# Kernel optimization log

Measured on AMD Instinct MI355X. Metric: run time of the kernel, lower is better.

The kernel has to match this reference:

```python
import jax, jax.numpy as jnp
import numpy as np

N = 500_000
K = 16
E = N * K
H = 256


def _linear_params(key, fan_in, fan_out):
    k1, k2 = jax.random.split(key)
    bound = 1.0 / np.sqrt(fan_in)
    W = jax.random.uniform(k1, (fan_in, fan_out), jnp.float32, -bound, bound)
    b = jax.random.uniform(k2, (fan_out,), jnp.float32, -bound, bound)
    return W, b


def setup_inputs() -> dict:
    key = jax.random.key(0)
    ks = jax.random.split(key, 10)
    x = jax.random.normal(ks[0], (N, 3), jnp.float32)
    edge_index = jax.random.randint(ks[1], (2, E), 0, N, jnp.int64)
    edge_attr = jax.random.normal(ks[2], (E, 1), jnp.float32)
    W1, b1 = _linear_params(ks[3], K, H)          # GNN1 message MLP: Linear(k, 256)
    We1, be1 = _linear_params(ks[4], H, 128)      # encoder Linear(256,128)
    We2, be2 = _linear_params(ks[5], 128, 6)      # encoder Linear(128,6)
    Wd1, bd1 = _linear_params(ks[6], 6, 128)      # decoder Linear(6,128)
    Wd2, bd2 = _linear_params(ks[7], 128, H)      # decoder Linear(128,256)
    Wo, bo = _linear_params(ks[8], H, 1)          # output Linear(256,1)
    return {"x": x, "edge_index": edge_index, "edge_attr": edge_attr,
            "W1": W1, "b1": b1, "We1": We1, "be1": be1, "We2": We2, "be2": be2,
            "Wd1": Wd1, "bd1": bd1, "Wd2": Wd2, "bd2": bd2, "Wo": Wo, "bo": bo}


def reference(x, edge_index, edge_attr, W1, b1, We1, be1, We2, be2,
              Wd1, bd1, Wd2, bd2, Wo, bo):
    # GNN1: messages are edge_attr verbatim (x_i/x_j ignored); aggregate reshapes
    # all E scalar messages into (N, k) (k edges per node, contiguous) and runs
    # Linear(k,256)+Tanh. Note: LSTM and GCN4 branches in the torch code are dead
    # (GNN1 ignores its node-feature input), so they do not affect the output.
    k = W1.shape[0]
    msgs = edge_attr.reshape(-1, k)                    # (N, k)
    h = jnp.tanh(msgs @ W1 + b1)                       # (N, 256)
    # second L1 call produces the identical result (depends only on edge_attr)
    z = jnp.tanh(jnp.tanh(h @ We1 + be1) @ We2 + be2)  # encoder -> (N, 6)
    d = jnp.tanh(z @ Wd1 + bd1) @ Wd2 + bd2            # decoder -> (N, 256)
    out = jax.nn.sigmoid(jnp.tanh(d) @ Wo + bo)        # (N, 1)
    return out[:, 0]                                   # squeeze(dim=1) -> (N,)
```

## Files before the change

kernel.cpp:

```cpp
#include <hip/hip_runtime.h>


#define N_NODES 500000

#define OFF_W1 0
#define OFF_W2 8192
#define OFF_W3 73728
#define OFF_W4 77824
#define OFF_W5 86016
#define OFF_WO 151552
#define OFF_B1 152576
#define OFF_B2 153600
#define OFF_B3 154112
#define OFF_B4 154176
#define OFF_B5 154688
#define IMG_BYTES 155712
#define IMG_ALLOC 156672

#define K1_LDS   79872
#define K1_B1    77824
#define K1_B2    78848
#define K1_B3    79360
#define K2_LDS   76800
#define K2_W4    0
#define K2_W5    8192
#define K2_WO    73728
#define K2_B4    74752
#define K2_B5    75264

typedef _Float16 half8  __attribute__((ext_vector_type(8)));
typedef __fp16   pk16x2 __attribute__((ext_vector_type(2)));
typedef float    f32x4  __attribute__((ext_vector_type(4)));
typedef int      int4v  __attribute__((ext_vector_type(4)));

__device__ __align__(16) char g_img[IMG_ALLOC];

static __device__ __forceinline__ unsigned pack_f16_rne(float a, float b) {
  _Float16 ha = (_Float16)a, hb = (_Float16)b;
  unsigned short ua = __builtin_bit_cast(unsigned short, ha);
  unsigned short ub = __builtin_bit_cast(unsigned short, hb);
  return (unsigned)ua | ((unsigned)ub << 16);
}
static __device__ __forceinline__ int pkrtz(float a, float b) {
  pk16x2 h = __builtin_amdgcn_cvt_pkrtz(a, b);
  return __builtin_bit_cast(int, h);
}
static __device__ __forceinline__ float tanh_f(float x) {
  float e = __builtin_amdgcn_exp2f(x * 2.8853900817779268f);
  float r = __builtin_amdgcn_rcpf(e + 1.0f);
  return __builtin_fmaf(-2.0f, r, 1.0f);
}
static __device__ __forceinline__ float sigmoid_f(float x) {
  float e = __builtin_amdgcn_exp2f(x * -1.4426950408889634f);
  return __builtin_amdgcn_rcpf(1.0f + e);
}
static __device__ __forceinline__ f32x4 mfma16(half8 a, int4v b, f32x4 c) {
  return __builtin_amdgcn_mfma_f32_16x16x32_f16(a, __builtin_bit_cast(half8, b), c, 0, 0, 0);
}
static __device__ __forceinline__ half8 lda(const char* smem, int off) {
  return *(const half8*)(smem + off);
}
static __device__ __forceinline__ f32x4 ldf4(const char* smem, int off) {
  return *(const f32x4*)(smem + off);
}
#define FENCE() __builtin_amdgcn_sched_barrier(0)

struct PK2 { int lo, hi; };
static __device__ __forceinline__ PK2 tp(f32x4 a) {
  PK2 p;
  p.lo = pkrtz(tanh_f(a.x), tanh_f(a.y));
  p.hi = pkrtz(tanh_f(a.z), tanh_f(a.w));
  return p;
}
static __device__ __forceinline__ int4v xform(PK2 e, PK2 o, int s1, int s2, bool qlo) {
  int x0 = __shfl(e.lo, s1, 64), y0 = __shfl(o.lo, s1, 64);
  int x1 = __shfl(e.hi, s1, 64), y1 = __shfl(o.hi, s1, 64);
  int x2 = __shfl(e.lo, s2, 64), y2 = __shfl(o.lo, s2, 64);
  int x3 = __shfl(e.hi, s2, 64), y3 = __shfl(o.hi, s2, 64);
  int4v r;
  r.x = qlo ? x0 : y0;  r.y = qlo ? x1 : y1;
  r.z = qlo ? x2 : y2;  r.w = qlo ? x3 : y3;
  return r;
}

__global__ void gnn_prep(const float* __restrict__ W1,  const float* __restrict__ b1,
                         const float* __restrict__ We1, const float* __restrict__ be1,
                         const float* __restrict__ We2, const float* __restrict__ be2,
                         const float* __restrict__ Wd1, const float* __restrict__ bd1,
                         const float* __restrict__ Wd2, const float* __restrict__ bd2,
                         const float* __restrict__ Wo)
{
  int t = blockIdx.x * 256 + threadIdx.x;
  int off = t * 4;
  if (off >= IMG_BYTES) return;
  unsigned val;
  if (off < OFF_W2) {
    int rel = off;
    int mi = rel >> 9, li = (rel >> 4) & 31, j2 = (rel >> 2) & 3;
    int fout = mi * 16 + (li & 15);
    int k0 = (li >> 4) * 8 + j2 * 2;
    val = pack_f16_rne(W1[k0 * 256 + fout], W1[(k0 + 1) * 256 + fout]);
  } else if (off < OFF_W3) {
    int rel = off - OFF_W2;
    int blk = rel >> 10, li = (rel >> 4) & 63, j2 = (rel >> 2) & 3;
    int mi = blk >> 3, ki = blk & 7;
    int fout = mi * 16 + (li & 15);
    int k0 = ki * 32 + (li >> 4) * 8 + j2 * 2;
    val = pack_f16_rne(We1[k0 * 128 + fout], We1[(k0 + 1) * 128 + fout]);
  } else if (off < OFF_W4) {
    int rel = off - OFF_W3;
    int ki = rel >> 10, li = (rel >> 4) & 63, j2 = (rel >> 2) & 3;
    int fo = li & 15;
    int k0 = ki * 32 + (li >> 4) * 8 + j2 * 2;
    float a = (fo < 6) ? We2[k0 * 6 + fo] : 0.0f;
    float b = (fo < 6) ? We2[(k0 + 1) * 6 + fo] : 0.0f;
    val = pack_f16_rne(a, b);
  } else if (off < OFF_W5) {
    int rel = off - OFF_W4;
    int mi = rel >> 10, li = (rel >> 4) & 63, j2 = (rel >> 2) & 3;
    int fout = mi * 16 + (li & 15);
    int k0 = (li >> 4) * 8 + j2 * 2;
    float a = (k0 < 6)     ? Wd1[k0 * 128 + fout]       : 0.0f;
    float b = (k0 + 1 < 6) ? Wd1[(k0 + 1) * 128 + fout] : 0.0f;
    val = pack_f16_rne(a, b);
  } else if (off < OFF_WO) {
    int rel = off - OFF_W5;
    int blk = rel >> 10, li = (rel >> 4) & 63, j2 = (rel >> 2) & 3;
    int mi = blk >> 2, ki = blk & 3;
    int fout = mi * 16 + (li & 15);
    int k0 = ki * 32 + (li >> 4) * 8 + j2 * 2;
    val = pack_f16_rne(Wd2[k0 * 256 + fout], Wd2[(k0 + 1) * 256 + fout]);
  } else if (off < OFF_B1) {
    val = __builtin_bit_cast(unsigned, Wo[(off - OFF_WO) >> 2]);
  } else if (off < OFF_B2) {
    val = __builtin_bit_cast(unsigned, b1[(off - OFF_B1) >> 2]);
  } else if (off < OFF_B3) {
    val = __builtin_bit_cast(unsigned, be1[(off - OFF_B2) >> 2]);
  } else if (off < OFF_B4) {
    int i = (off - OFF_B3) >> 2;
    float v = (i < 6) ? be2[i] : 0.0f;
    val = __builtin_bit_cast(unsigned, v);
  } else if (off < OFF_B5) {
    val = __builtin_bit_cast(unsigned, bd1[(off - OFF_B4) >> 2]);
  } else {
    val = __builtin_bit_cast(unsigned, bd2[(off - OFF_B5) >> 2]);
  }
  *(unsigned*)(g_img + off) = val;
}

static __device__ __forceinline__ void stage_chunk(const char* src, char* dst) {
  __builtin_amdgcn_global_load_lds(
      (const __attribute__((address_space(1))) void*)src,
      (__attribute__((address_space(3))) void*)dst, 16, 0, 0);
}

#define L1_PAIR(KO, OUT_G0, OUT_G1) do {                                   \
    half8 Ae = lda(smem, OFF_W1 + (2*(KO))*512 + (ln & 31)*16);            \
    half8 Ao = lda(smem, OFF_W1 + (2*(KO)+1)*512 + (ln & 31)*16);          \
    if (!qlo) { Ae = h8z; Ao = h8z; }                                      \
    f32x4 be_ = ldf4(smem, K1_B1 + (2*(KO))*64 + q*16);                    \
    f32x4 bo_ = ldf4(smem, K1_B1 + (2*(KO)+1)*64 + q*16);                  \
    f32x4 ae0 = mfma16(Ae, b1g0, be_);                                     \
    f32x4 ae1 = mfma16(Ae, b1g1, be_);                                     \
    f32x4 ao0 = mfma16(Ao, b1g0, bo_);                                     \
    f32x4 ao1 = mfma16(Ao, b1g1, bo_);                                     \
    PK2 pe0 = tp(ae0), po0 = tp(ao0), pe1 = tp(ae1), po1 = tp(ao1);        \
    OUT_G0 = xform(pe0, po0, s1, s2, qlo);                                 \
    OUT_G1 = xform(pe1, po1, s1, s2, qlo);                                 \
    FENCE();                                                               \
  } while (0)

#define L2_MI(MI, ACC0, ACC1) do {                                                            \
    f32x4 bb = ldf4(smem, K1_B2 + (MI)*64 + q*16);                                            \
    ACC0 = bb; ACC1 = bb;                                                                     \
    half8 A;                                                                                  \
    A = lda(smem, OFF_W2 + ((MI)*8+0)*1024 + ln*16); ACC0 = mfma16(A, c2g0_0, ACC0); ACC1 = mfma16(A, c2g1_0, ACC1); \
    A = lda(smem, OFF_W2 + ((MI)*8+1)*1024 + ln*16); ACC0 = mfma16(A, c2g0_1, ACC0); ACC1 = mfma16(A, c2g1_1, ACC1); \
    A = lda(smem, OFF_W2 + ((MI)*8+2)*1024 + ln*16); ACC0 = mfma16(A, c2g0_2, ACC0); ACC1 = mfma16(A, c2g1_2, ACC1); \
    A = lda(smem, OFF_W2 + ((MI)*8+3)*1024 + ln*16); ACC0 = mfma16(A, c2g0_3, ACC0); ACC1 = mfma16(A, c2g1_3, ACC1); \
    A = lda(smem, OFF_W2 + ((MI)*8+4)*1024 + ln*16); ACC0 = mfma16(A, c2g0_4, ACC0); ACC1 = mfma16(A, c2g1_4, ACC1); \
    A = lda(smem, OFF_W2 + ((MI)*8+5)*1024 + ln*16); ACC0 = mfma16(A, c2g0_5, ACC0); ACC1 = mfma16(A, c2g1_5, ACC1); \
    A = lda(smem, OFF_W2 + ((MI)*8+6)*1024 + ln*16); ACC0 = mfma16(A, c2g0_6, ACC0); ACC1 = mfma16(A, c2g1_6, ACC1); \
    A = lda(smem, OFF_W2 + ((MI)*8+7)*1024 + ln*16); ACC0 = mfma16(A, c2g0_7, ACC0); ACC1 = mfma16(A, c2g1_7, ACC1); \
  } while (0)

#define L2_PAIR(KO, OUT_G0, OUT_G1) do {                                   \
    f32x4 ve0, ve1, vo0, vo1;                                              \
    L2_MI(2*(KO),   ve0, ve1);                                             \
    FENCE();                                                               \
    L2_MI(2*(KO)+1, vo0, vo1);                                             \
    PK2 pe0 = tp(ve0), po0 = tp(vo0), pe1 = tp(ve1), po1 = tp(vo1);        \
    OUT_G0 = xform(pe0, po0, s1, s2, qlo);                                 \
    OUT_G1 = xform(pe1, po1, s1, s2, qlo);                                 \
    FENCE();                                                               \
  } while (0)

__global__ __launch_bounds__(512)
void gnn_k1(const float* __restrict__ ea, int4v* __restrict__ zbuf)
{
  __shared__ __align__(16) char smem[K1_LDS];
  const int tid = threadIdx.x;
  const int wv = tid >> 6, ln = tid & 63;

#pragma unroll 1
  for (int r = 0; r < 10; ++r) {
    int cb = (r * 8 + wv) << 6;
    if (cb < 4992) {
      int src = (cb < 4864) ? cb * 16 : OFF_B1 + (cb - 4864) * 16;
      stage_chunk(g_img + src + ln * 16, smem + (size_t)cb * 16 + ln * 16);
    }
  }
  __syncthreads();

  const int q = ln >> 4, c = ln & 15;
  const bool qlo = (q < 2);
  const int s1 = ((q & 1) << 5) + c;
  const int s2 = s1 + 16;
  const int4v zi4 = {0, 0, 0, 0};
  const half8 h8z = __builtin_bit_cast(half8, zi4);

  const int NT = (N_NODES + 255) / 256;
#pragma unroll 1
  for (int t = blockIdx.x; t < NT; t += gridDim.x) {
    const int base = t * 256 + wv * 32;

    int nl = base + (q >> 1) * 16 + c;
    if (nl > N_NODES - 1) nl = N_NODES - 1;
    const f32x4* ea4 = (const f32x4*)ea;
    size_t eb = (size_t)nl * 4 + (size_t)((q & 1) * 2);
    f32x4 vlo = ea4[eb];
    f32x4 vhi = ea4[eb + 1];
    int p0 = pkrtz(vlo.x, vlo.y), p1 = pkrtz(vlo.z, vlo.w);
    int p2 = pkrtz(vhi.x, vhi.y), p3 = pkrtz(vhi.z, vhi.w);
    int4v b1g0, b1g1;
    b1g0.x = qlo ? p0 : 0; b1g0.y = qlo ? p1 : 0;
    b1g0.z = qlo ? p2 : 0; b1g0.w = qlo ? p3 : 0;
    int sh = (ln + 32) & 63;
    int r0 = __shfl(p0, sh, 64), r1 = __shfl(p1, sh, 64);
    int r2 = __shfl(p2, sh, 64), r3 = __shfl(p3, sh, 64);
    b1g1.x = qlo ? r0 : 0; b1g1.y = qlo ? r1 : 0;
    b1g1.z = qlo ? r2 : 0; b1g1.w = qlo ? r3 : 0;

    int4v c2g0_0, c2g0_1, c2g0_2, c2g0_3, c2g0_4, c2g0_5, c2g0_6, c2g0_7;
    int4v c2g1_0, c2g1_1, c2g1_2, c2g1_3, c2g1_4, c2g1_5, c2g1_6, c2g1_7;
    L1_PAIR(0, c2g0_0, c2g1_0);
    L1_PAIR(1, c2g0_1, c2g1_1);
    L1_PAIR(2, c2g0_2, c2g1_2);
    L1_PAIR(3, c2g0_3, c2g1_3);
    L1_PAIR(4, c2g0_4, c2g1_4);
    L1_PAIR(5, c2g0_5, c2g1_5);
    L1_PAIR(6, c2g0_6, c2g1_6);
    L1_PAIR(7, c2g0_7, c2g1_7);

    int4v c3g0_0, c3g0_1, c3g0_2, c3g0_3;
    int4v c3g1_0, c3g1_1, c3g1_2, c3g1_3;
    L2_PAIR(0, c3g0_0, c3g1_0);
    L2_PAIR(1, c3g0_1, c3g1_1);
    L2_PAIR(2, c3g0_2, c3g1_2);
    L2_PAIR(3, c3g0_3, c3g1_3);

    f32x4 bb3 = ldf4(smem, K1_B3 + q * 16);
    f32x4 z0 = bb3, z1 = bb3;
    half8 A;
    A = lda(smem, OFF_W3 + 0 * 1024 + ln * 16); z0 = mfma16(A, c3g0_0, z0); z1 = mfma16(A, c3g1_0, z1);
    A = lda(smem, OFF_W3 + 1 * 1024 + ln * 16); z0 = mfma16(A, c3g0_1, z0); z1 = mfma16(A, c3g1_1, z1);
    A = lda(smem, OFF_W3 + 2 * 1024 + ln * 16); z0 = mfma16(A, c3g0_2, z0); z1 = mfma16(A, c3g1_2, z1);
    A = lda(smem, OFF_W3 + 3 * 1024 + ln * 16); z0 = mfma16(A, c3g0_3, z0); z1 = mfma16(A, c3g1_3, z1);
    PK2 p3g0 = tp(z0);
    PK2 p3g1 = tp(z1);

    if (ln < 32) {
      int4v zv;
      zv.x = p3g0.lo; zv.y = p3g0.hi; zv.z = p3g1.lo; zv.w = p3g1.hi;
      zbuf[(size_t)(t * 8 + wv) * 32 + ln] = zv;
    }
  }
}

#define L4_MI(MI, ACC0, ACC1) do {                                         \
    f32x4 bb = ldf4(smem, K2_B4 + (MI)*64 + q*16);                         \
    half8 A = lda(smem, K2_W4 + (MI)*1024 + ln*16);                        \
    ACC0 = mfma16(A, b4g0, bb);                                            \
    ACC1 = mfma16(A, b4g1, bb);                                            \
  } while (0)

#define L4_PAIR(KO, OUT_G0, OUT_G1) do {                                   \
    f32x4 ve0, ve1, vo0, vo1;                                              \
    L4_MI(2*(KO),   ve0, ve1);                                             \
    L4_MI(2*(KO)+1, vo0, vo1);                                             \
    PK2 pe0 = tp(ve0), po0 = tp(vo0), pe1 = tp(ve1), po1 = tp(vo1);        \
    OUT_G0 = xform(pe0, po0, s1, s2, qlo);                                 \
    OUT_G1 = xform(pe1, po1, s1, s2, qlo);                                 \
    FENCE();                                                               \
  } while (0)

#define L5_MI(MI) do {                                                                        \
    f32x4 bb = ldf4(smem, K2_B5 + (MI)*64 + q*16);                                            \
    f32x4 a0 = bb, a1 = bb;                                                                   \
    half8 A;                                                                                  \
    A = lda(smem, K2_W5 + ((MI)*4+0)*1024 + ln*16); a0 = mfma16(A, c5g0_0, a0); a1 = mfma16(A, c5g1_0, a1); \
    A = lda(smem, K2_W5 + ((MI)*4+1)*1024 + ln*16); a0 = mfma16(A, c5g0_1, a0); a1 = mfma16(A, c5g1_1, a1); \
    A = lda(smem, K2_W5 + ((MI)*4+2)*1024 + ln*16); a0 = mfma16(A, c5g0_2, a0); a1 = mfma16(A, c5g1_2, a1); \
    A = lda(smem, K2_W5 + ((MI)*4+3)*1024 + ln*16); a0 = mfma16(A, c5g0_3, a0); a1 = mfma16(A, c5g1_3, a1); \
    f32x4 wo = ldf4(smem, K2_WO + (MI)*64 + q*16);                                            \
    part0 += tanh_f(a0.x)*wo.x + tanh_f(a0.y)*wo.y + tanh_f(a0.z)*wo.z + tanh_f(a0.w)*wo.w;   \
    part1 += tanh_f(a1.x)*wo.x + tanh_f(a1.y)*wo.y + tanh_f(a1.z)*wo.z + tanh_f(a1.w)*wo.w;   \
    FENCE();                                                                                  \
  } while (0)

__global__ __launch_bounds__(512)
void gnn_k2(const int4v* __restrict__ zbuf, float* __restrict__ out,
            const float* __restrict__ bo_p)
{
  __shared__ __align__(16) char smem[K2_LDS];
  const int tid = threadIdx.x;
  const int wv = tid >> 6, ln = tid & 63;

#pragma unroll 1
  for (int r = 0; r < 10; ++r) {
    int cb = (r * 8 + wv) << 6;
    if (cb < 4800) {
      int src;
      if (cb < 512)       src = OFF_W4 + cb * 16;
      else if (cb < 4672) src = OFF_W5 + (cb - 512) * 16;
      else                src = OFF_B4 + (cb - 4672) * 16;
      stage_chunk(g_img + src + ln * 16, smem + (size_t)cb * 16 + ln * 16);
    }
  }
  __syncthreads();

  const int q = ln >> 4, c = ln & 15;
  const bool qlo = (q < 2);
  const int s1 = ((q & 1) << 5) + c;
  const int s2 = s1 + 16;
  const float bo = *bo_p;

  const int NT = (N_NODES + 255) / 256;
#pragma unroll 1
  for (int t = blockIdx.x; t < NT; t += gridDim.x) {
    const int base = t * 256 + wv * 32;

    int4v zv = {0, 0, 0, 0};
    if (ln < 32) zv = zbuf[(size_t)(t * 8 + wv) * 32 + ln];
    PK2 p3g0, p3g1;
    p3g0.lo = zv.x; p3g0.hi = zv.y; p3g1.lo = zv.z; p3g1.hi = zv.w;

    int4v b4g0, b4g1;
    {
      int a0 = __shfl(p3g0.lo, s1, 64), a1 = __shfl(p3g0.hi, s1, 64);
      int a2 = __shfl(p3g0.lo, s2, 64), a3 = __shfl(p3g0.hi, s2, 64);
      b4g0.x = qlo ? a0 : 0; b4g0.y = qlo ? a1 : 0;
      b4g0.z = qlo ? a2 : 0; b4g0.w = qlo ? a3 : 0;
      int d0 = __shfl(p3g1.lo, s1, 64), d1 = __shfl(p3g1.hi, s1, 64);
      int d2 = __shfl(p3g1.lo, s2, 64), d3 = __shfl(p3g1.hi, s2, 64);
      b4g1.x = qlo ? d0 : 0; b4g1.y = qlo ? d1 : 0;
      b4g1.z = qlo ? d2 : 0; b4g1.w = qlo ? d3 : 0;
    }

    int4v c5g0_0, c5g0_1, c5g0_2, c5g0_3;
    int4v c5g1_0, c5g1_1, c5g1_2, c5g1_3;
    L4_PAIR(0, c5g0_0, c5g1_0);
    L4_PAIR(1, c5g0_1, c5g1_1);
    L4_PAIR(2, c5g0_2, c5g1_2);
    L4_PAIR(3, c5g0_3, c5g1_3);

    float part0 = 0.0f, part1 = 0.0f;
    L5_MI(0);  L5_MI(1);  L5_MI(2);  L5_MI(3);
    L5_MI(4);  L5_MI(5);  L5_MI(6);  L5_MI(7);
    L5_MI(8);  L5_MI(9);  L5_MI(10); L5_MI(11);
    L5_MI(12); L5_MI(13); L5_MI(14); L5_MI(15);

    part0 += __shfl_xor(part0, 16, 64); part0 += __shfl_xor(part0, 32, 64);
    part1 += __shfl_xor(part1, 16, 64); part1 += __shfl_xor(part1, 32, 64);
    if (q < 2) {
      int node = base + q * 16 + c;
      if (node < N_NODES) {
        float v = ((q == 0) ? part0 : part1) + bo;
        out[node] = sigmoid_f(v);
      }
    }
  }
}

extern "C" void kernel_launch(void* const* d_in, const int* in_sizes, int n_in,
                              void* d_out, int out_size, void* d_ws, size_t ws_size,
                              hipStream_t stream) {
  (void)in_sizes; (void)n_in; (void)ws_size; (void)out_size;
  const float* ea  = (const float*)d_in[2];
  const float* W1  = (const float*)d_in[3];
  const float* b1  = (const float*)d_in[4];
  const float* We1 = (const float*)d_in[5];
  const float* be1 = (const float*)d_in[6];
  const float* We2 = (const float*)d_in[7];
  const float* be2 = (const float*)d_in[8];
  const float* Wd1 = (const float*)d_in[9];
  const float* bd1 = (const float*)d_in[10];
  const float* Wd2 = (const float*)d_in[11];
  const float* bd2 = (const float*)d_in[12];
  const float* Wo  = (const float*)d_in[13];
  const float* bo  = (const float*)d_in[14];

  gnn_prep<<<dim3((IMG_BYTES / 4 + 255) / 256), dim3(256), 0, stream>>>(
      W1, b1, We1, be1, We2, be2, Wd1, bd1, Wd2, bd2, Wo);
  gnn_k1<<<dim3(512), dim3(512), 0, stream>>>(ea, (int4v*)d_ws);
  gnn_k2<<<dim3(512), dim3(512), 0, stream>>>((const int4v*)d_ws, (float*)d_out, bo);
}
```

Before: 262.0 us.

## Permute weight K-layout so MFMA outputs feed next layer without shuffles

Reorders the K index mapping of the packed f16 weight images (We1, We2, Wd1, Wd2) so that the accumulator layout of one 16x16x32 MFMA matches the B-operand layout the next layer expects. This removes the cross-lane __shfl transpose (xform) between layers, along with the shuffle-based unpacking of the latent z, replacing them with plain register moves. It cuts many ds_bpermute operations per layer, in exchange for a more intricate weight packing that must stay consistent with the MFMA operand layout.

```diff
diff --git a/kernel.cpp b/kernel.cpp
--- a/kernel.cpp
+++ b/kernel.cpp
@@ -71,16 +71,6 @@
   p.lo = pkrtz(tanh_f(a.x), tanh_f(a.y));
   p.hi = pkrtz(tanh_f(a.z), tanh_f(a.w));
   return p;
-}
-static __device__ __forceinline__ int4v xform(PK2 e, PK2 o, int s1, int s2, bool qlo) {
-  int x0 = __shfl(e.lo, s1, 64), y0 = __shfl(o.lo, s1, 64);
-  int x1 = __shfl(e.hi, s1, 64), y1 = __shfl(o.hi, s1, 64);
-  int x2 = __shfl(e.lo, s2, 64), y2 = __shfl(o.lo, s2, 64);
-  int x3 = __shfl(e.hi, s2, 64), y3 = __shfl(o.hi, s2, 64);
-  int4v r;
-  r.x = qlo ? x0 : y0;  r.y = qlo ? x1 : y1;
-  r.z = qlo ? x2 : y2;  r.w = qlo ? x3 : y3;
-  return r;
 }
 
 __global__ void gnn_prep(const float* __restrict__ W1,  const float* __restrict__ b1,
@@ -105,13 +95,13 @@
     int blk = rel >> 10, li = (rel >> 4) & 63, j2 = (rel >> 2) & 3;
     int mi = blk >> 3, ki = blk & 7;
     int fout = mi * 16 + (li & 15);
-    int k0 = ki * 32 + (li >> 4) * 8 + j2 * 2;
+    int k0 = ki * 32 + 4 * (li >> 4) + 16 * (j2 >> 1) + 2 * (j2 & 1);
     val = pack_f16_rne(We1[k0 * 128 + fout], We1[(k0 + 1) * 128 + fout]);
   } else if (off < OFF_W4) {
     int rel = off - OFF_W3;
     int ki = rel >> 10, li = (rel >> 4) & 63, j2 = (rel >> 2) & 3;
     int fo = li & 15;
-    int k0 = ki * 32 + (li >> 4) * 8 + j2 * 2;
+    int k0 = ki * 32 + 4 * (li >> 4) + 16 * (j2 >> 1) + 2 * (j2 & 1);
     float a = (fo < 6) ? We2[k0 * 6 + fo] : 0.0f;
     float b = (fo < 6) ? We2[(k0 + 1) * 6 + fo] : 0.0f;
     val = pack_f16_rne(a, b);
@@ -119,16 +109,21 @@
     int rel = off - OFF_W4;
     int mi = rel >> 10, li = (rel >> 4) & 63, j2 = (rel >> 2) & 3;
     int fout = mi * 16 + (li & 15);
-    int k0 = (li >> 4) * 8 + j2 * 2;
-    float a = (k0 < 6)     ? Wd1[k0 * 128 + fout]       : 0.0f;
-    float b = (k0 + 1 < 6) ? Wd1[(k0 + 1) * 128 + fout] : 0.0f;
-    val = pack_f16_rne(a, b);
+    int qa = li >> 4;
+    unsigned v = 0;
+    if (j2 < 2) {
+      int k0 = 4 * qa + 2 * j2;
+      float a = (k0 < 6)     ? Wd1[k0 * 128 + fout]       : 0.0f;
+      float b = (k0 + 1 < 6) ? Wd1[(k0 + 1) * 128 + fout] : 0.0f;
+      v = pack_f16_rne(a, b);
+    }
+    val = v;
   } else if (off < OFF_WO) {
     int rel = off - OFF_W5;
     int blk = rel >> 10, li = (rel >> 4) & 63, j2 = (rel >> 2) & 3;
     int mi = blk >> 2, ki = blk & 3;
     int fout = mi * 16 + (li & 15);
-    int k0 = ki * 32 + (li >> 4) * 8 + j2 * 2;
+    int k0 = ki * 32 + 4 * (li >> 4) + 16 * (j2 >> 1) + 2 * (j2 & 1);
     val = pack_f16_rne(Wd2[k0 * 256 + fout], Wd2[(k0 + 1) * 256 + fout]);
   } else if (off < OFF_B1) {
     val = __builtin_bit_cast(unsigned, Wo[(off - OFF_WO) >> 2]);
@@ -165,8 +160,8 @@
     f32x4 ao0 = mfma16(Ao, b1g0, bo_);                                     \
     f32x4 ao1 = mfma16(Ao, b1g1, bo_);                                     \
     PK2 pe0 = tp(ae0), po0 = tp(ao0), pe1 = tp(ae1), po1 = tp(ao1);        \
-    OUT_G0 = xform(pe0, po0, s1, s2, qlo);                                 \
-    OUT_G1 = xform(pe1, po1, s1, s2, qlo);                                 \
+    OUT_G0.x = pe0.lo; OUT_G0.y = pe0.hi; OUT_G0.z = po0.lo; OUT_G0.w = po0.hi; \
+    OUT_G1.x = pe1.lo; OUT_G1.y = pe1.hi; OUT_G1.z = po1.lo; OUT_G1.w = po1.hi; \
     FENCE();                                                               \
   } while (0)
 
@@ -190,8 +185,8 @@
     FENCE();                                                               \
     L2_MI(2*(KO)+1, vo0, vo1);                                             \
     PK2 pe0 = tp(ve0), po0 = tp(vo0), pe1 = tp(ve1), po1 = tp(vo1);        \
-    OUT_G0 = xform(pe0, po0, s1, s2, qlo);                                 \
-    OUT_G1 = xform(pe1, po1, s1, s2, qlo);                                 \
+    OUT_G0.x = pe0.lo; OUT_G0.y = pe0.hi; OUT_G0.z = po0.lo; OUT_G0.w = po0.hi; \
+    OUT_G1.x = pe1.lo; OUT_G1.y = pe1.hi; OUT_G1.z = po1.lo; OUT_G1.w = po1.hi; \
     FENCE();                                                               \
   } while (0)
 
@@ -214,8 +209,6 @@
 
   const int q = ln >> 4, c = ln & 15;
   const bool qlo = (q < 2);
-  const int s1 = ((q & 1) << 5) + c;
-  const int s2 = s1 + 16;
   const int4v zi4 = {0, 0, 0, 0};
   const half8 h8z = __builtin_bit_cast(half8, zi4);
 
@@ -289,8 +282,8 @@
     L4_MI(2*(KO),   ve0, ve1);                                             \
     L4_MI(2*(KO)+1, vo0, vo1);                                             \
     PK2 pe0 = tp(ve0), po0 = tp(vo0), pe1 = tp(ve1), po1 = tp(vo1);        \
-    OUT_G0 = xform(pe0, po0, s1, s2, qlo);                                 \
-    OUT_G1 = xform(pe1, po1, s1, s2, qlo);                                 \
+    OUT_G0.x = pe0.lo; OUT_G0.y = pe0.hi; OUT_G0.z = po0.lo; OUT_G0.w = po0.hi; \
+    OUT_G1.x = pe1.lo; OUT_G1.y = pe1.hi; OUT_G1.z = po1.lo; OUT_G1.w = po1.hi; \
     FENCE();                                                               \
   } while (0)
 
@@ -330,9 +323,6 @@
   __syncthreads();
 
   const int q = ln >> 4, c = ln & 15;
-  const bool qlo = (q < 2);
-  const int s1 = ((q & 1) << 5) + c;
-  const int s2 = s1 + 16;
   const float bo = *bo_p;
 
   const int NT = (N_NODES + 255) / 256;
@@ -342,20 +332,10 @@
 
     int4v zv = {0, 0, 0, 0};
     if (ln < 32) zv = zbuf[(size_t)(t * 8 + wv) * 32 + ln];
-    PK2 p3g0, p3g1;
-    p3g0.lo = zv.x; p3g0.hi = zv.y; p3g1.lo = zv.z; p3g1.hi = zv.w;
 
     int4v b4g0, b4g1;
-    {
-      int a0 = __shfl(p3g0.lo, s1, 64), a1 = __shfl(p3g0.hi, s1, 64);
-      int a2 = __shfl(p3g0.lo, s2, 64), a3 = __shfl(p3g0.hi, s2, 64);
-      b4g0.x = qlo ? a0 : 0; b4g0.y = qlo ? a1 : 0;
-      b4g0.z = qlo ? a2 : 0; b4g0.w = qlo ? a3 : 0;
-      int d0 = __shfl(p3g1.lo, s1, 64), d1 = __shfl(p3g1.hi, s1, 64);
-      int d2 = __shfl(p3g1.lo, s2, 64), d3 = __shfl(p3g1.hi, s2, 64);
-      b4g1.x = qlo ? d0 : 0; b4g1.y = qlo ? d1 : 0;
-      b4g1.z = qlo ? d2 : 0; b4g1.w = qlo ? d3 : 0;
-    }
+    b4g0.x = zv.x; b4g0.y = zv.y; b4g0.z = 0; b4g0.w = 0;
+    b4g1.x = zv.z; b4g1.y = zv.w; b4g1.z = 0; b4g1.w = 0;
 
     int4v c5g0_0, c5g0_1, c5g0_2, c5g0_3;
     int4v c5g1_0, c5g1_1, c5g1_2, c5g1_3;
```

New measurement: 249.3 us. 4.9% less time.
